# Kernel tuning notes

Measured on AMD Instinct MI355X. Metric: run time of the kernel, lower is better.

The kernel has to match this reference:

```python
import jax, jax.numpy as jnp
import numpy as np

WIN_H = WIN_W = 7
NUM_HEADS = 6
DIM = 192
HEAD_DIM = DIM // NUM_HEADS
NUM_WIN = 1024
B_ = 8192
N = WIN_H * WIN_W


def _relative_position_index(win_h, win_w):
    coords = np.stack(np.meshgrid(np.arange(win_h), np.arange(win_w), indexing='ij'))  # (2,h,w)
    flat = coords.reshape(2, -1)
    rel = flat[:, :, None] - flat[:, None, :]          # (2, N, N)
    rel = rel.transpose(1, 2, 0).astype(np.int32)      # (N, N, 2)
    rel[:, :, 0] += win_h - 1
    rel[:, :, 1] += win_w - 1
    rel[:, :, 0] *= 2 * win_w - 1
    return rel.sum(-1)                                 # (N, N) in [0, (2h-1)(2w-1))


def setup_inputs() -> dict:
    key = jax.random.key(0)
    ks = jax.random.split(key, 7)
    return {
        'x': jax.random.normal(ks[0], (B_, N, DIM), jnp.float32),
        'mask': jax.random.normal(ks[1], (NUM_WIN, N, N), jnp.float32),
        'qkv_w': jax.random.normal(ks[2], (3 * DIM, DIM), jnp.float32) * 0.02,
        'qkv_b': jax.random.normal(ks[3], (3 * DIM,), jnp.float32) * 0.02,
        'proj_w': jax.random.normal(ks[4], (DIM, DIM), jnp.float32) * 0.02,
        'proj_b': jax.random.normal(ks[5], (DIM,), jnp.float32) * 0.02,
        'rpb_table': jax.random.normal(ks[6], ((2 * WIN_H - 1) * (2 * WIN_W - 1), NUM_HEADS), jnp.float32) * 0.02,
        'rel_index': jnp.asarray(_relative_position_index(WIN_H, WIN_W)),
    }


def reference(x, mask, qkv_w, qkv_b, proj_w, proj_b, rpb_table, rel_index):
    B, n, C = x.shape
    H, hd = NUM_HEADS, HEAD_DIM
    scale = hd ** (-0.5)

    qkv = (x @ qkv_w.T + qkv_b).reshape(B, n, 3, H, hd)
    qkv = jnp.transpose(qkv, (2, 0, 3, 1, 4))          # (3, B, H, N, hd)
    q, k, v = qkv[0], qkv[1], qkv[2]

    attn = jnp.einsum('bhnd,bhmd->bhnm', q * scale, k)  # (B, H, N, N)

    # gathered relative position bias: (N*N,) -> (N, N, H) -> (H, N, N)
    bias = rpb_table[rel_index.reshape(-1)].reshape(n, n, H)
    attn = attn + jnp.transpose(bias, (2, 0, 1))[None]

    num_win = mask.shape[0]
    attn = attn.reshape(B // num_win, num_win, H, n, n) + mask[None, :, None]
    attn = jax.nn.softmax(attn, axis=-1).reshape(B, H, n, n)

    out = jnp.einsum('bhnm,bhmd->bhnd', attn, v)         # (B, H, N, hd)
    out = jnp.transpose(out, (0, 2, 1, 3)).reshape(B, n, H * hd)
    return out @ proj_w.T + proj_b
```

## Files before the change

kernel.cpp:

```cpp
#include <hip/hip_runtime.h>

#define NTOK  49
#define NWIN  1024
#define SCALE 0.17677669529663687f

#define SMEM_BYTES 102400

typedef __bf16 bfx8 __attribute__((ext_vector_type(8)));
typedef float  f32x4 __attribute__((ext_vector_type(4)));
typedef unsigned long long ull;

union BF8 { bfx8 v; ull q[2]; };

__device__ __forceinline__ unsigned short f2bf(float f) {
    unsigned int u = __builtin_bit_cast(unsigned int, f);
    u += 0x7fffu + ((u >> 16) & 1u);
    return (unsigned short)(u >> 16);
}
__device__ __forceinline__ ull pack4(f32x4 a) {
    return (ull)f2bf(a[0]) | ((ull)f2bf(a[1]) << 16) |
           ((ull)f2bf(a[2]) << 32) | ((ull)f2bf(a[3]) << 48);
}

extern "C" __global__ void wattn_prep(const float* __restrict__ qkv_w,
                                      const float* __restrict__ proj_w,
                                      const float* __restrict__ rpb,
                                      const int*   __restrict__ rel,
                                      const float* __restrict__ qkv_b,
                                      unsigned short* __restrict__ W1f,
                                      unsigned short* __restrict__ W2p,
                                      float* __restrict__ qkvbs,
                                      float* __restrict__ biasN)
{
    const int i = blockIdx.x * 256 + threadIdx.x;
    if (i < 110592) {
        const int e = i & 7, l = (i >> 3) & 63, f = i >> 9;
        const int kk = f % 6, oct = f / 6;
        const int R = oct * 16 + (l & 15), C = kk * 32 + (l >> 4) * 8 + e;
        float v = qkv_w[R * 192 + C];
        if (oct < 12) v *= SCALE;
        W1f[i] = f2bf(v);
    }
    if (i < 36864) {
        const int e = i & 7, l = (i >> 3) & 63, f = i >> 9;
        const int c2t = f / 6, H = f % 6;
        const int R = c2t * 16 + (l & 15);
        const int C = H * 32 + (e >> 2) * 16 + (l >> 4) * 4 + (e & 3);
        W2p[i] = f2bf(proj_w[R * 192 + C]);
    }
    if (i < 576) qkvbs[i] = (i < 192) ? qkv_b[i] * SCALE : qkv_b[i];
    if (i < 6 * NTOK * 64) {
        const int h = i / (NTOK * 64), ii = (i / 64) % NTOK, j = i % 64;
        biasN[i] = (j < NTOK) ? rpb[rel[ii * NTOK + j] * 6 + h] : 0.f;
    }
}

extern "C" __global__ void __launch_bounds__(512, 2)
wattn_fused(const float* __restrict__ x,
            const float* __restrict__ mask,
            const float* __restrict__ proj_b,
            const unsigned short* __restrict__ W1f,
            const unsigned short* __restrict__ W2p,
            const float* __restrict__ qkvbs,
            const float* __restrict__ biasN,
            float* __restrict__ out)
{
    __shared__ char smem[SMEM_BYTES];
    char* const XB  = smem;
    char* const OBX = smem;
    char* const QBp = smem + 25600;
    char* const KBp = smem + 50176;
    char* const VTp = smem + 74752;

    const int tid  = threadIdx.x;
    const int wave = tid >> 6;
    const int lane = tid & 63;
    const int g    = lane >> 4;
    const int jn   = lane & 15;
    const int qt   = wave & 3;
    const int hh   = wave >> 2;
    const size_t b = blockIdx.x;

#pragma unroll
    for (int u = 0; u < 3; ++u) {
        const int i = tid + u * 512;
        if (i < 1500)
            *(unsigned int*)(XB + (49 + i / 100) * 400 + (i % 100) * 4) = 0u;
    }
    {
        const float4* xw = (const float4*)(x + b * 9408);
#pragma unroll
        for (int u = 0; u < 5; ++u) {
            const int i = tid + u * 512;
            if (i < 2352) {
                float4 v = xw[i];
                *(ull*)(XB + (i / 48) * 400 + (i % 48) * 8) =
                    (ull)f2bf(v.x) | ((ull)f2bf(v.y) << 16) |
                    ((ull)f2bf(v.z) << 32) | ((ull)f2bf(v.w) << 48);
            }
        }
    }
    __syncthreads();

    for (int oct = wave; oct < 36; oct += 8) {
        bfx8 wf_[6];
#pragma unroll
        for (int kk = 0; kk < 6; ++kk)
            wf_[kk] = *(const bfx8*)(W1f + ((size_t)(oct * 6 + kk) * 64 + lane) * 8);
        if (oct < 24) {
            const f32x4 binit = *(const f32x4*)(qkvbs + oct * 16 + 4 * g);
            char* const dst = (oct < 12) ? QBp : KBp;
            const int ct12 = (oct < 12) ? oct : oct - 12;
#pragma unroll
            for (int tt = 0; tt < 4; ++tt) {
                f32x4 acc = binit;
#pragma unroll
                for (int kk = 0; kk < 6; ++kk) {
                    bfx8 xf = *(const bfx8*)(XB + (tt * 16 + jn) * 400 + kk * 64 + g * 16);
                    acc = __builtin_amdgcn_mfma_f32_16x16x32_bf16(wf_[kk], xf, acc, 0, 0, 0);
                }
                *(ull*)(dst + ((tt * 6 + (ct12 >> 1)) * 64 + lane) * 16 + (ct12 & 1) * 8) = pack4(acc);
            }
        } else {
            const float bv = qkvbs[oct * 16 + jn];
            const int ct12 = oct - 24;
#pragma unroll
            for (int tt = 0; tt < 4; ++tt) {
                f32x4 acc = {bv, bv, bv, bv};
#pragma unroll
                for (int kk = 0; kk < 6; ++kk) {
                    bfx8 xf = *(const bfx8*)(XB + (tt * 16 + jn) * 400 + kk * 64 + g * 16);
                    acc = __builtin_amdgcn_mfma_f32_16x16x32_bf16(xf, wf_[kk], acc, 0, 0, 0);
                }
                *(ull*)(VTp + (ct12 * 16 + jn) * 144 + (tt >> 1) * 64 + g * 16 + (tt & 1) * 8) = pack4(acc);
            }
        }
    }
    __syncthreads();

    const int iq = qt * 16 + jn;
    const int ic = iq < NTOK ? iq : NTOK - 1;
    const float* mw = mask + (b & (NWIN - 1)) * (NTOK * NTOK);
    float mv[4][4];
#pragma unroll
    for (int kt = 0; kt < 4; ++kt)
#pragma unroll
        for (int r = 0; r < 4; ++r) {
            const int j = kt * 16 + 4 * g + r;
            const int jc = j < NTOK ? j : NTOK - 1;
            mv[kt][r] = mw[ic * NTOK + jc];
        }

#pragma unroll
    for (int hl = 0; hl < 3; ++hl) {
        const int H = hh * 3 + hl;
        bfx8 qfr = *(const bfx8*)(QBp + ((qt * 6 + H) * 64 + lane) * 16);
        f32x4 p[4];
#pragma unroll
        for (int kt = 0; kt < 4; ++kt) {
            bfx8 kf = *(const bfx8*)(KBp + ((kt * 6 + H) * 64 + lane) * 16);
            f32x4 z = {0.f, 0.f, 0.f, 0.f};
            p[kt] = __builtin_amdgcn_mfma_f32_16x16x32_bf16(kf, qfr, z, 0, 0, 0);
        }
        float mx = -1e30f;
#pragma unroll
        for (int kt = 0; kt < 4; ++kt) {
            const f32x4 bm4 = *(const f32x4*)(biasN + ((size_t)H * NTOK + ic) * 64 + kt * 16 + 4 * g);
#pragma unroll
            for (int r = 0; r < 4; ++r) {
                const int j = kt * 16 + 4 * g + r;
                const float v = (j < NTOK) ? p[kt][r] + bm4[r] + mv[kt][r] : -1e30f;
                p[kt][r] = v;
                mx = fmaxf(mx, v);
            }
        }
        mx = fmaxf(mx, __shfl_xor(mx, 16));
        mx = fmaxf(mx, __shfl_xor(mx, 32));
        float sum = 0.f;
#pragma unroll
        for (int kt = 0; kt < 4; ++kt)
#pragma unroll
            for (int r = 0; r < 4; ++r) {
                p[kt][r] = __expf(p[kt][r] - mx);
                sum += p[kt][r];
            }
        sum += __shfl_xor(sum, 16);
        sum += __shfl_xor(sum, 32);
        const float inv = 1.f / sum;
        BF8 p01, p23;
        p01.q[0] = pack4(p[0]); p01.q[1] = pack4(p[1]);
        p23.q[0] = pack4(p[2]); p23.q[1] = pack4(p[3]);
#pragma unroll
        for (int ct = 0; ct < 2; ++ct) {
            const int row = H * 32 + ct * 16 + jn;
            bfx8 v0 = *(const bfx8*)(VTp + row * 144 + g * 16);
            bfx8 v1 = *(const bfx8*)(VTp + row * 144 + 64 + g * 16);
            f32x4 o = {0.f, 0.f, 0.f, 0.f};
            o = __builtin_amdgcn_mfma_f32_16x16x32_bf16(v0, p01.v, o, 0, 0, 0);
            o = __builtin_amdgcn_mfma_f32_16x16x32_bf16(v1, p23.v, o, 0, 0, 0);
            *(ull*)(OBX + ((qt * 6 + H) * 64 + lane) * 16 + ct * 8) = pack4(o * inv);
        }
    }
    __syncthreads();

    float* outp = out + b * 9408;
    for (int c2t = wave; c2t < 12; c2t += 8) {
        bfx8 wf2[6];
#pragma unroll
        for (int H = 0; H < 6; ++H)
            wf2[H] = *(const bfx8*)(W2p + ((size_t)(c2t * 6 + H) * 64 + lane) * 8);
        const f32x4 pb = *(const f32x4*)(proj_b + c2t * 16 + 4 * g);
#pragma unroll
        for (int qt2 = 0; qt2 < 4; ++qt2) {
            f32x4 acc = pb;
#pragma unroll
            for (int H = 0; H < 6; ++H) {
                bfx8 ob = *(const bfx8*)(OBX + ((qt2 * 6 + H) * 64 + lane) * 16);
                acc = __builtin_amdgcn_mfma_f32_16x16x32_bf16(wf2[H], ob, acc, 0, 0, 0);
            }
            const int tok = qt2 * 16 + jn;
            if (tok < NTOK)
                *(f32x4*)(outp + tok * 192 + c2t * 16 + 4 * g) = acc;
        }
    }
}

extern "C" void kernel_launch(void* const* d_in, const int* in_sizes, int n_in,
                              void* d_out, int out_size, void* d_ws, size_t ws_size,
                              hipStream_t stream) {
    const float* x      = (const float*)d_in[0];
    const float* mask   = (const float*)d_in[1];
    const float* qkv_w  = (const float*)d_in[2];
    const float* qkv_b  = (const float*)d_in[3];
    const float* proj_w = (const float*)d_in[4];
    const float* proj_b = (const float*)d_in[5];
    const float* rpb    = (const float*)d_in[6];
    const int*   rel    = (const int*)d_in[7];
    float* outp = (float*)d_out;

    char* ws = (char*)d_ws;
    unsigned short* W1f = (unsigned short*)ws;
    unsigned short* W2p = (unsigned short*)(ws + 221184);
    float* qkvbs        = (float*)(ws + 221184 + 73728);
    float* biasN        = (float*)(ws + 221184 + 73728 + 2304);

    wattn_prep<<<432, 256, 0, stream>>>(qkv_w, proj_w, rpb, rel, qkv_b,
                                        W1f, W2p, qkvbs, biasN);
    wattn_fused<<<8192, 512, 0, stream>>>(x, mask, proj_b,
                                          W1f, W2p, qkvbs, biasN, outp);
}
```

Before: 456.5 us.

## Stage mask and bf16 bias in LDS, prefetch weights, balance tail work

Mask rows are loaded with coalesced reads into padded LDS during the x load, instead of strided per-lane global gathers in the softmax phase. The relative-position bias table is now stored in bf16 with a padded row stride and copied into LDS per block. The first QKV and projection weight fragments are prefetched before barriers. The leftover V-projection octets and the output projection are split so all 8 waves get equal work. This raises LDS use to about 149KB, which still fits one block per CU, and rounding the bias to bf16 adds a small precision loss.

```diff
diff --git a/kernel.cpp b/kernel.cpp
--- a/kernel.cpp
+++ b/kernel.cpp
@@ -4,18 +4,25 @@
 #define NWIN  1024
 #define SCALE 0.17677669529663687f
 
-#define SMEM_BYTES 102400
+#define LDS_MSK 102400
+#define LDS_BSB 112640
+#define SMEM_BYTES 152640
 
 typedef __bf16 bfx8 __attribute__((ext_vector_type(8)));
 typedef float  f32x4 __attribute__((ext_vector_type(4)));
 typedef unsigned long long ull;
+typedef unsigned int uint;
 
 union BF8 { bfx8 v; ull q[2]; };
 
 __device__ __forceinline__ unsigned short f2bf(float f) {
-    unsigned int u = __builtin_bit_cast(unsigned int, f);
+    uint u = __builtin_bit_cast(uint, f);
     u += 0x7fffu + ((u >> 16) & 1u);
     return (unsigned short)(u >> 16);
+}
+__device__ __forceinline__ float bf2f(uint u16) {
+    uint x = (u16 & 0xffffu) << 16;
+    return __builtin_bit_cast(float, x);
 }
 __device__ __forceinline__ ull pack4(f32x4 a) {
     return (ull)f2bf(a[0]) | ((ull)f2bf(a[1]) << 16) |
@@ -30,7 +37,7 @@
                                       unsigned short* __restrict__ W1f,
                                       unsigned short* __restrict__ W2p,
                                       float* __restrict__ qkvbs,
-                                      float* __restrict__ biasN)
+                                      unsigned short* __restrict__ biasB)
 {
     const int i = blockIdx.x * 256 + threadIdx.x;
     if (i < 110592) {
@@ -49,9 +56,9 @@
         W2p[i] = f2bf(proj_w[R * 192 + C]);
     }
     if (i < 576) qkvbs[i] = (i < 192) ? qkv_b[i] * SCALE : qkv_b[i];
-    if (i < 6 * NTOK * 64) {
-        const int h = i / (NTOK * 64), ii = (i / 64) % NTOK, j = i % 64;
-        biasN[i] = (j < NTOK) ? rpb[rel[ii * NTOK + j] * 6 + h] : 0.f;
+    if (i < 6 * NTOK * 68) {
+        const int h = i / (NTOK * 68), ii = (i / 68) % NTOK, j = i % 68;
+        biasB[i] = (j < NTOK) ? f2bf(rpb[rel[ii * NTOK + j] * 6 + h]) : 0;
     }
 }
 
@@ -62,7 +69,7 @@
             const unsigned short* __restrict__ W1f,
             const unsigned short* __restrict__ W2p,
             const float* __restrict__ qkvbs,
-            const float* __restrict__ biasN,
+            const unsigned short* __restrict__ biasB,
             float* __restrict__ out)
 {
     __shared__ char smem[SMEM_BYTES];
@@ -71,6 +78,8 @@
     char* const QBp = smem + 25600;
     char* const KBp = smem + 50176;
     char* const VTp = smem + 74752;
+    char* const MSK = smem + LDS_MSK;
+    char* const BSB = smem + LDS_BSB;
 
     const int tid  = threadIdx.x;
     const int wave = tid >> 6;
@@ -78,14 +87,18 @@
     const int g    = lane >> 4;
     const int jn   = lane & 15;
     const int qt   = wave & 3;
-    const int hh   = wave >> 2;
     const size_t b = blockIdx.x;
+
+    bfx8 wfp[6];
+#pragma unroll
+    for (int kk = 0; kk < 6; ++kk)
+        wfp[kk] = *(const bfx8*)(W1f + ((size_t)(wave * 6 + kk) * 64 + lane) * 8);
 
 #pragma unroll
     for (int u = 0; u < 3; ++u) {
         const int i = tid + u * 512;
         if (i < 1500)
-            *(unsigned int*)(XB + (49 + i / 100) * 400 + (i % 100) * 4) = 0u;
+            *(uint*)(XB + (49 + i / 100) * 400 + (i % 100) * 4) = 0u;
     }
     {
         const float4* xw = (const float4*)(x + b * 9408);
@@ -100,13 +113,34 @@
             }
         }
     }
+    {
+        const float* mw = mask + (b & (NWIN - 1)) * (NTOK * NTOK);
+#pragma unroll
+        for (int u = 0; u < 5; ++u) {
+            const int i = tid + u * 512;
+            if (i < NTOK * NTOK)
+                *(float*)(MSK + ((i / 49) * 52 + (i % 49)) * 4) = mw[i];
+        }
+    }
+    {
+        const uint* bsrc = (const uint*)biasB;
+        uint* bdst = (uint*)BSB;
+#pragma unroll
+        for (int u = 0; u < 20; ++u) {
+            const int i = tid + u * 512;
+            if (i < 9996) bdst[i] = bsrc[i];
+        }
+    }
     __syncthreads();
 
-    for (int oct = wave; oct < 36; oct += 8) {
+#pragma unroll
+    for (int jj = 0; jj < 4; ++jj) {
+        const int oct = wave + 8 * jj;
         bfx8 wf_[6];
 #pragma unroll
         for (int kk = 0; kk < 6; ++kk)
-            wf_[kk] = *(const bfx8*)(W1f + ((size_t)(oct * 6 + kk) * 64 + lane) * 8);
+            wf_[kk] = (jj == 0) ? wfp[kk]
+                    : *(const bfx8*)(W1f + ((size_t)(oct * 6 + kk) * 64 + lane) * 8);
         if (oct < 24) {
             const f32x4 binit = *(const f32x4*)(qkvbs + oct * 16 + 4 * g);
             char* const dst = (oct < 12) ? QBp : KBp;
@@ -136,20 +170,36 @@
             }
         }
     }
+    {
+        const int oct = 32 + (wave >> 1);
+        const int ct12 = oct - 24;
+        const int ttb = (wave & 1) * 2;
+        bfx8 wf_[6];
+#pragma unroll
+        for (int kk = 0; kk < 6; ++kk)
+            wf_[kk] = *(const bfx8*)(W1f + ((size_t)(oct * 6 + kk) * 64 + lane) * 8);
+        const float bv = qkvbs[oct * 16 + jn];
+#pragma unroll
+        for (int t2 = 0; t2 < 2; ++t2) {
+            const int tt = ttb + t2;
+            f32x4 acc = {bv, bv, bv, bv};
+#pragma unroll
+            for (int kk = 0; kk < 6; ++kk) {
+                bfx8 xf = *(const bfx8*)(XB + (tt * 16 + jn) * 400 + kk * 64 + g * 16);
+                acc = __builtin_amdgcn_mfma_f32_16x16x32_bf16(xf, wf_[kk], acc, 0, 0, 0);
+            }
+            *(ull*)(VTp + (ct12 * 16 + jn) * 144 + (tt >> 1) * 64 + g * 16 + (tt & 1) * 8) = pack4(acc);
+        }
+    }
     __syncthreads();
 
+    const int hh = wave >> 2;
     const int iq = qt * 16 + jn;
     const int ic = iq < NTOK ? iq : NTOK - 1;
-    const float* mw = mask + (b & (NWIN - 1)) * (NTOK * NTOK);
-    float mv[4][4];
+    f32x4 mv4[4];
 #pragma unroll
     for (int kt = 0; kt < 4; ++kt)
-#pragma unroll
-        for (int r = 0; r < 4; ++r) {
-            const int j = kt * 16 + 4 * g + r;
-            const int jc = j < NTOK ? j : NTOK - 1;
-            mv[kt][r] = mw[ic * NTOK + jc];
-        }
+        mv4[kt] = *(const f32x4*)(MSK + ic * 208 + kt * 64 + g * 16);
 
 #pragma unroll
     for (int hl = 0; hl < 3; ++hl) {
@@ -165,11 +215,12 @@
         float mx = -1e30f;
 #pragma unroll
         for (int kt = 0; kt < 4; ++kt) {
-            const f32x4 bm4 = *(const f32x4*)(biasN + ((size_t)H * NTOK + ic) * 64 + kt * 16 + 4 * g);
+            const ull bq = *(const ull*)(BSB + ((size_t)(H * NTOK + ic)) * 136 + kt * 32 + g * 8);
 #pragma unroll
             for (int r = 0; r < 4; ++r) {
                 const int j = kt * 16 + 4 * g + r;
-                const float v = (j < NTOK) ? p[kt][r] + bm4[r] + mv[kt][r] : -1e30f;
+                const float v = (j < NTOK)
+                    ? p[kt][r] + bf2f((uint)(bq >> (16 * r))) + mv4[kt][r] : -1e30f;
                 p[kt][r] = v;
                 mx = fmaxf(mx, v);
             }
@@ -201,17 +252,28 @@
             *(ull*)(OBX + ((qt * 6 + H) * 64 + lane) * 16 + ct * 8) = pack4(o * inv);
         }
     }
+
+    bfx8 wf2p[6];
+#pragma unroll
+    for (int H = 0; H < 6; ++H)
+        wf2p[H] = *(const bfx8*)(W2p + ((size_t)((wave >> 1) * 6 + H) * 64 + lane) * 8);
     __syncthreads();
 
     float* outp = out + b * 9408;
-    for (int c2t = wave; c2t < 12; c2t += 8) {
+#pragma unroll
+    for (int t = 0; t < 3; ++t) {
+        const int j = wave + 8 * t;
+        const int c2t = j >> 1;
+        const int qh  = j & 1;
         bfx8 wf2[6];
 #pragma unroll
         for (int H = 0; H < 6; ++H)
-            wf2[H] = *(const bfx8*)(W2p + ((size_t)(c2t * 6 + H) * 64 + lane) * 8);
+            wf2[H] = (t == 0) ? wf2p[H]
+                   : *(const bfx8*)(W2p + ((size_t)(c2t * 6 + H) * 64 + lane) * 8);
         const f32x4 pb = *(const f32x4*)(proj_b + c2t * 16 + 4 * g);
 #pragma unroll
-        for (int qt2 = 0; qt2 < 4; ++qt2) {
+        for (int t2 = 0; t2 < 2; ++t2) {
+            const int qt2 = qh * 2 + t2;
             f32x4 acc = pb;
 #pragma unroll
             for (int H = 0; H < 6; ++H) {
@@ -239,13 +301,13 @@
     float* outp = (float*)d_out;
 
     char* ws = (char*)d_ws;
-    unsigned short* W1f = (unsigned short*)ws;
-    unsigned short* W2p = (unsigned short*)(ws + 221184);
-    float* qkvbs        = (float*)(ws + 221184 + 73728);
-    float* biasN        = (float*)(ws + 221184 + 73728 + 2304);
+    unsigned short* W1f   = (unsigned short*)ws;
+    unsigned short* W2p   = (unsigned short*)(ws + 221184);
+    float* qkvbs          = (float*)(ws + 221184 + 73728);
+    unsigned short* biasB = (unsigned short*)(ws + 221184 + 73728 + 2304);
 
     wattn_prep<<<432, 256, 0, stream>>>(qkv_w, proj_w, rpb, rel, qkv_b,
-                                        W1f, W2p, qkvbs, biasN);
+                                        W1f, W2p, qkvbs, biasB);
     wattn_fused<<<8192, 512, 0, stream>>>(x, mask, proj_b,
-                                          W1f, W2p, qkvbs, biasN, outp);
-}
+                                          W1f, W2p, qkvbs, biasB, outp);
+}
```

Measured after the change: 461.1 us. No clear change (+1.0%).

## Rebalance QKV and projection GEMM work across waves and pair output tiles

Applied to the files above, without the earlier changes.

The QKV projection now gives each wave pairs of adjacent 16-column tiles. Two independent MFMA chains interleave and share each X fragment load, and Q/K results go out as single 16-byte stores. The leftover V tiles are spread so all 8 waves do equal work, and the output projection is split into 24 half-tiles so all waves are busy instead of 4 idling. Padding columns of the bias table are set to -1e30 so the per-element mask check in softmax can be dropped. In exchange the weight fragments held per wave double, raising register pressure under the 2-blocks-per-CU launch bound.

```diff
diff --git a/kernel.cpp b/kernel.cpp
--- a/kernel.cpp
+++ b/kernel.cpp
@@ -9,17 +9,21 @@
 typedef __bf16 bfx8 __attribute__((ext_vector_type(8)));
 typedef float  f32x4 __attribute__((ext_vector_type(4)));
 typedef unsigned long long ull;
+typedef unsigned int uint;
 
 union BF8 { bfx8 v; ull q[2]; };
 
 __device__ __forceinline__ unsigned short f2bf(float f) {
-    unsigned int u = __builtin_bit_cast(unsigned int, f);
+    uint u = __builtin_bit_cast(uint, f);
     u += 0x7fffu + ((u >> 16) & 1u);
     return (unsigned short)(u >> 16);
 }
 __device__ __forceinline__ ull pack4(f32x4 a) {
     return (ull)f2bf(a[0]) | ((ull)f2bf(a[1]) << 16) |
            ((ull)f2bf(a[2]) << 32) | ((ull)f2bf(a[3]) << 48);
+}
+__device__ __forceinline__ f32x4 mfma16(bfx8 a, bfx8 b, f32x4 c) {
+    return __builtin_amdgcn_mfma_f32_16x16x32_bf16(a, b, c, 0, 0, 0);
 }
 
 extern "C" __global__ void wattn_prep(const float* __restrict__ qkv_w,
@@ -51,7 +55,7 @@
     if (i < 576) qkvbs[i] = (i < 192) ? qkv_b[i] * SCALE : qkv_b[i];
     if (i < 6 * NTOK * 64) {
         const int h = i / (NTOK * 64), ii = (i / 64) % NTOK, j = i % 64;
-        biasN[i] = (j < NTOK) ? rpb[rel[ii * NTOK + j] * 6 + h] : 0.f;
+        biasN[i] = (j < NTOK) ? rpb[rel[ii * NTOK + j] * 6 + h] : -1e30f;
     }
 }
 
@@ -85,7 +89,7 @@
     for (int u = 0; u < 3; ++u) {
         const int i = tid + u * 512;
         if (i < 1500)
-            *(unsigned int*)(XB + (49 + i / 100) * 400 + (i % 100) * 4) = 0u;
+            *(uint*)(XB + (49 + i / 100) * 400 + (i % 100) * 4) = 0u;
     }
     {
         const float4* xw = (const float4*)(x + b * 9408);
@@ -102,39 +106,77 @@
     }
     __syncthreads();
 
-    for (int oct = wave; oct < 36; oct += 8) {
-        bfx8 wf_[6];
-#pragma unroll
-        for (int kk = 0; kk < 6; ++kk)
-            wf_[kk] = *(const bfx8*)(W1f + ((size_t)(oct * 6 + kk) * 64 + lane) * 8);
-        if (oct < 24) {
-            const f32x4 binit = *(const f32x4*)(qkvbs + oct * 16 + 4 * g);
-            char* const dst = (oct < 12) ? QBp : KBp;
-            const int ct12 = (oct < 12) ? oct : oct - 12;
+#pragma unroll
+    for (int jj = 0; jj < 2; ++jj) {
+        const int pr = wave + 8 * jj;
+        const int octA = pr * 2;
+        bfx8 wfA[6], wfB[6];
+#pragma unroll
+        for (int kk = 0; kk < 6; ++kk) {
+            wfA[kk] = *(const bfx8*)(W1f + ((size_t)(octA * 6 + kk) * 64 + lane) * 8);
+            wfB[kk] = *(const bfx8*)(W1f + ((size_t)((octA + 1) * 6 + kk) * 64 + lane) * 8);
+        }
+        if (pr < 12) {
+            const f32x4 biA = *(const f32x4*)(qkvbs + octA * 16 + 4 * g);
+            const f32x4 biB = *(const f32x4*)(qkvbs + (octA + 1) * 16 + 4 * g);
+            char* const dst = (pr < 6) ? QBp : KBp;
+            const int pp = (pr < 6) ? pr : pr - 6;
 #pragma unroll
             for (int tt = 0; tt < 4; ++tt) {
-                f32x4 acc = binit;
+                f32x4 aA = biA, aB = biB;
 #pragma unroll
                 for (int kk = 0; kk < 6; ++kk) {
                     bfx8 xf = *(const bfx8*)(XB + (tt * 16 + jn) * 400 + kk * 64 + g * 16);
-                    acc = __builtin_amdgcn_mfma_f32_16x16x32_bf16(wf_[kk], xf, acc, 0, 0, 0);
+                    aA = mfma16(wfA[kk], xf, aA);
+                    aB = mfma16(wfB[kk], xf, aB);
                 }
-                *(ull*)(dst + ((tt * 6 + (ct12 >> 1)) * 64 + lane) * 16 + (ct12 & 1) * 8) = pack4(acc);
+                BF8 o; o.q[0] = pack4(aA); o.q[1] = pack4(aB);
+                *(bfx8*)(dst + ((tt * 6 + pp) * 64 + lane) * 16) = o.v;
             }
         } else {
-            const float bv = qkvbs[oct * 16 + jn];
-            const int ct12 = oct - 24;
+            const float bvA = qkvbs[octA * 16 + jn];
+            const float bvB = qkvbs[(octA + 1) * 16 + jn];
+            const int cA = octA - 24;
 #pragma unroll
             for (int tt = 0; tt < 4; ++tt) {
-                f32x4 acc = {bv, bv, bv, bv};
+                f32x4 aA = {bvA, bvA, bvA, bvA};
+                f32x4 aB = {bvB, bvB, bvB, bvB};
 #pragma unroll
                 for (int kk = 0; kk < 6; ++kk) {
                     bfx8 xf = *(const bfx8*)(XB + (tt * 16 + jn) * 400 + kk * 64 + g * 16);
-                    acc = __builtin_amdgcn_mfma_f32_16x16x32_bf16(xf, wf_[kk], acc, 0, 0, 0);
+                    aA = mfma16(xf, wfA[kk], aA);
+                    aB = mfma16(xf, wfB[kk], aB);
                 }
-                *(ull*)(VTp + (ct12 * 16 + jn) * 144 + (tt >> 1) * 64 + g * 16 + (tt & 1) * 8) = pack4(acc);
-            }
-        }
+                const int voff = (tt >> 1) * 64 + g * 16 + (tt & 1) * 8;
+                *(ull*)(VTp + (cA * 16 + jn) * 144 + voff)       = pack4(aA);
+                *(ull*)(VTp + ((cA + 1) * 16 + jn) * 144 + voff) = pack4(aB);
+            }
+        }
+        __builtin_amdgcn_sched_barrier(0);
+    }
+    {
+        const int octA = 32 + (wave >> 2) * 2;
+        const int tt = wave & 3;
+        bfx8 wfA[6], wfB[6];
+#pragma unroll
+        for (int kk = 0; kk < 6; ++kk) {
+            wfA[kk] = *(const bfx8*)(W1f + ((size_t)(octA * 6 + kk) * 64 + lane) * 8);
+            wfB[kk] = *(const bfx8*)(W1f + ((size_t)((octA + 1) * 6 + kk) * 64 + lane) * 8);
+        }
+        const float bvA = qkvbs[octA * 16 + jn];
+        const float bvB = qkvbs[(octA + 1) * 16 + jn];
+        f32x4 aA = {bvA, bvA, bvA, bvA};
+        f32x4 aB = {bvB, bvB, bvB, bvB};
+#pragma unroll
+        for (int kk = 0; kk < 6; ++kk) {
+            bfx8 xf = *(const bfx8*)(XB + (tt * 16 + jn) * 400 + kk * 64 + g * 16);
+            aA = mfma16(xf, wfA[kk], aA);
+            aB = mfma16(xf, wfB[kk], aB);
+        }
+        const int cA = octA - 24;
+        const int voff = (tt >> 1) * 64 + g * 16 + (tt & 1) * 8;
+        *(ull*)(VTp + (cA * 16 + jn) * 144 + voff)       = pack4(aA);
+        *(ull*)(VTp + ((cA + 1) * 16 + jn) * 144 + voff) = pack4(aB);
     }
     __syncthreads();
 
@@ -160,7 +202,7 @@
         for (int kt = 0; kt < 4; ++kt) {
             bfx8 kf = *(const bfx8*)(KBp + ((kt * 6 + H) * 64 + lane) * 16);
             f32x4 z = {0.f, 0.f, 0.f, 0.f};
-            p[kt] = __builtin_amdgcn_mfma_f32_16x16x32_bf16(kf, qfr, z, 0, 0, 0);
+            p[kt] = mfma16(kf, qfr, z);
         }
         float mx = -1e30f;
 #pragma unroll
@@ -168,8 +210,7 @@
             const f32x4 bm4 = *(const f32x4*)(biasN + ((size_t)H * NTOK + ic) * 64 + kt * 16 + 4 * g);
 #pragma unroll
             for (int r = 0; r < 4; ++r) {
-                const int j = kt * 16 + 4 * g + r;
-                const float v = (j < NTOK) ? p[kt][r] + bm4[r] + mv[kt][r] : -1e30f;
+                const float v = p[kt][r] + bm4[r] + mv[kt][r];
                 p[kt][r] = v;
                 mx = fmaxf(mx, v);
             }
@@ -196,27 +237,32 @@
             bfx8 v0 = *(const bfx8*)(VTp + row * 144 + g * 16);
             bfx8 v1 = *(const bfx8*)(VTp + row * 144 + 64 + g * 16);
             f32x4 o = {0.f, 0.f, 0.f, 0.f};
-            o = __builtin_amdgcn_mfma_f32_16x16x32_bf16(v0, p01.v, o, 0, 0, 0);
-            o = __builtin_amdgcn_mfma_f32_16x16x32_bf16(v1, p23.v, o, 0, 0, 0);
+            o = mfma16(v0, p01.v, o);
+            o = mfma16(v1, p23.v, o);
             *(ull*)(OBX + ((qt * 6 + H) * 64 + lane) * 16 + ct * 8) = pack4(o * inv);
         }
     }
     __syncthreads();
 
     float* outp = out + b * 9408;
-    for (int c2t = wave; c2t < 12; c2t += 8) {
+#pragma unroll
+    for (int t = 0; t < 3; ++t) {
+        const int j = wave + 8 * t;
+        const int c2t = j >> 1;
+        const int qh  = j & 1;
         bfx8 wf2[6];
 #pragma unroll
         for (int H = 0; H < 6; ++H)
             wf2[H] = *(const bfx8*)(W2p + ((size_t)(c2t * 6 + H) * 64 + lane) * 8);
         const f32x4 pb = *(const f32x4*)(proj_b + c2t * 16 + 4 * g);
 #pragma unroll
-        for (int qt2 = 0; qt2 < 4; ++qt2) {
+        for (int t2 = 0; t2 < 2; ++t2) {
+            const int qt2 = qh * 2 + t2;
             f32x4 acc = pb;
 #pragma unroll
             for (int H = 0; H < 6; ++H) {
                 bfx8 ob = *(const bfx8*)(OBX + ((qt2 * 6 + H) * 64 + lane) * 16);
-                acc = __builtin_amdgcn_mfma_f32_16x16x32_bf16(wf2[H], ob, acc, 0, 0, 0);
+                acc = mfma16(wf2[H], ob, acc);
             }
             const int tok = qt2 * 16 + jn;
             if (tok < NTOK)
```

Result: faster. 431.6 us (-5.5%).
